# Optimization experiments

Measured on AMD Instinct MI355X. Metric: run time of the kernel, lower is better.

The kernel has to match this reference:

```python
import jax, jax.numpy as jnp
import numpy as np

B, S, E, H = 4, 8192, 1024, 16
D = E // H  # head_dim = 64


def setup_inputs() -> dict:
    key = jax.random.key(0)
    ks = jax.random.split(key, 6)
    x = jax.random.normal(ks[0], (B, S, E), dtype=jnp.float32)
    key_padding_mask = jax.random.randint(ks[1], (B, S), 0, 2).astype(jnp.bool_)
    scale = 1.0 / np.sqrt(E)
    Wq = jax.random.normal(ks[2], (E, E), dtype=jnp.float32) * scale
    Wk = jax.random.normal(ks[3], (E, E), dtype=jnp.float32) * scale
    Wv = jax.random.normal(ks[4], (E, E), dtype=jnp.float32) * scale
    Wo = jax.random.normal(ks[5], (E, E), dtype=jnp.float32) * scale
    return {"x": x, "key_padding_mask": key_padding_mask,
            "Wq": Wq, "Wk": Wk, "Wv": Wv, "Wo": Wo}


def reference(x, key_padding_mask, Wq, Wk, Wv, Wo):
    b, s, _ = x.shape
    # torch Linear (no bias): y = x @ W.T
    Q = (x @ Wq.T).reshape(b, s, H, D).transpose(0, 2, 1, 3)  # (b,h,s,d)
    K = (x @ Wk.T).reshape(b, s, H, D).transpose(0, 2, 1, 3)
    V = (x @ Wv.T).reshape(b, s, H, D).transpose(0, 2, 1, 3)
    Q = jax.nn.elu(Q) + 1.0
    K = jax.nn.elu(K) + 1.0
    mask = key_padding_mask[:, None, :, None]  # (b,1,s,1), True = padding
    K = jnp.where(mask, 0.0, K)
    V = jnp.where(mask, 0.0, V)
    # global KV summarization over sequence: (b,h,d,e)
    KV = jnp.einsum('bhsd,bhse->bhde', K, V)
    K_sum = K.sum(axis=2)  # (b,h,d)
    Z = 1.0 / (jnp.einsum('bhsd,bhd->bhs', Q, K_sum) + 1e-6)  # (b,h,s)
    out = jnp.einsum('bhsd,bhde->bhse', Q, KV) * Z[..., None]  # (b,h,s,e)
    out = out.transpose(0, 2, 1, 3).reshape(b, s, E)
    return out @ Wo.T
```

## Files before the change

### kernel.cpp

```cpp
#include <hip/hip_runtime.h>

#define NB 4
#define NS 8192
#define NE 1024
#define NH 16
#define ND 64
#define NM (NB*NS)
#define NKT 16

typedef __bf16 bf16x8 __attribute__((ext_vector_type(8)));
typedef float  f32x4  __attribute__((ext_vector_type(4)));
typedef unsigned short u16x8 __attribute__((ext_vector_type(8)));

__device__ __forceinline__ unsigned short f2bf(float f){
  unsigned int u = __float_as_uint(f);
  u += 0x7FFFu + ((u >> 16) & 1u);
  return (unsigned short)(u >> 16);
}
__device__ __forceinline__ float bf2f(unsigned short h){
  return __uint_as_float(((unsigned int)h) << 16);
}
__device__ __forceinline__ void gload16(const void* g, void* lds){
  __builtin_amdgcn_global_load_lds(
      (__attribute__((address_space(1))) unsigned int*)g,
      (__attribute__((address_space(3))) unsigned int*)lds, 16, 0, 0);
}

__global__ void mask_prep(const void* mraw, unsigned char* mask_u8){
  __shared__ int flag_s;
  if (threadIdx.x == 0) flag_s = 0;
  __syncthreads();
  const unsigned int* mi = (const unsigned int*)mraw;
  int bad = 0;
  for (int i = threadIdx.x; i < 4096; i += 256) bad |= (mi[i] > 1u) ? 1 : 0;
  if (bad) atomicOr(&flag_s, 1);
  __syncthreads();
  const int isbyte = flag_s;
  const unsigned char* mb = (const unsigned char*)mraw;
  int stride = gridDim.x * blockDim.x;
  for (int i = blockIdx.x*blockDim.x + threadIdx.x; i < NM; i += stride)
    mask_u8[i] = isbyte ? (unsigned char)(mb[i] != 0) : (unsigned char)(mi[i] != 0);
}

struct CastJobs {
  const float* src[5];
  unsigned short* dst[5];
  int n4[5];
};

__global__ __launch_bounds__(256) void castk(CastJobs J){
  int j = blockIdx.y;
  const float* s = J.src[j];
  unsigned short* d = J.dst[j];
  int n4 = J.n4[j];
  int stride = gridDim.x * blockDim.x;
  for (int i = blockIdx.x*blockDim.x + threadIdx.x; i < n4; i += stride){
    float4 v = *(const float4*)(s + (long)i*4);
    ushort4 o;
    o.x = f2bf(v.x); o.y = f2bf(v.y); o.z = f2bf(v.z); o.w = f2bf(v.w);
    *(ushort4*)(d + (long)i*4) = o;
  }
}

__global__ __launch_bounds__(512, 2) void gemm256(
    const unsigned short* __restrict__ A,
    const unsigned short* __restrict__ W0,
    const unsigned short* __restrict__ W1,
    const unsigned short* __restrict__ W2,
    unsigned short* __restrict__ O0,
    unsigned short* __restrict__ O1,
    unsigned short* __restrict__ O2,
    float* __restrict__ OF,
    const unsigned char* __restrict__ mask,
    int modeSel)
{
  __shared__ __align__(16) unsigned short As[2*256*64];
  __shared__ __align__(16) unsigned short Bs[2*256*64];

  const int mode = (modeSel < 0) ? (int)blockIdx.y : modeSel;
  const unsigned short* Bw = (mode==0) ? W0 : (mode==1) ? W1 : (mode==2) ? W2 : W0;
  unsigned short* Obf = (mode==0) ? O0 : (mode==1) ? O1 : O2;

  const int nwg = (int)gridDim.x;
  const int bx  = (int)blockIdx.x;
  const int swz = (bx & 7) * (nwg >> 3) + (bx >> 3);
  const long m0 = (long)(swz >> 2) * 256;
  const int  n0 = (swz & 3) * 256;

  const int tid = (int)threadIdx.x;
  const int l   = tid & 63;
  const int wv  = tid >> 6;
  const int wr  = wv >> 2;
  const int wc  = wv & 3;
  const int l15 = l & 15;
  const int lhi = l >> 4;
  const int swz8 = (l & 7) * 8;

  const int srow = wv*16 + (l >> 3);
  const int scol = ((l & 7) * 8) ^ ((l >> 3) << 3);

  auto stageA = [&](int st, int h){
    if (st >= NKT) return;
    const long col = (long)st*64 + scol;
    #pragma unroll
    for (int is = 0; is < 2; ++is)
      gload16(A + (m0 + h*128 + srow + is*8)*NE + col,
              &As[(st & 1)*16384 + h*8192 + (wv*2 + is)*512]);
  };
  auto stageB = [&](int st, int h){
    if (st >= NKT) return;
    const long col = (long)st*64 + scol;
    #pragma unroll
    for (int is = 0; is < 2; ++is)
      gload16(Bw + (long)(n0 + h*128 + srow + is*8)*NE + col,
              &Bs[(st & 1)*16384 + h*8192 + (wv*2 + is)*512]);
  };

  auto lda = [&](int buf, int mi, int ks)->bf16x8 {
    const int row = wr*128 + mi*16 + l15;
    const int col = (ks*32 + lhi*8) ^ swz8;
    return *(const bf16x8*)&As[buf*16384 + row*64 + col];
  };
  auto ldb = [&](int buf, int ni, int ks)->bf16x8 {
    const int row = wc*64 + ni*16 + l15;
    const int col = (ks*32 + lhi*8) ^ swz8;
    return *(const bf16x8*)&Bs[buf*16384 + row*64 + col];
  };

  f32x4 acc[8][4];
  #pragma unroll
  for (int i=0;i<8;++i)
    #pragma unroll
    for (int j=0;j<4;++j)
      acc[i][j] = (f32x4){0.f,0.f,0.f,0.f};

  stageA(0,0); stageA(0,1); stageB(0,0); stageB(0,1);
  stageA(1,0); stageA(1,1); stageB(1,0); stageB(1,1);
  asm volatile("s_waitcnt vmcnt(8)" ::: "memory");
  __builtin_amdgcn_s_barrier();

  bf16x8 a0[4][2], a1[4][2], b0[2][2], b1[2][2];

  #pragma unroll 2
  for (int kt = 0; kt < NKT; ++kt){
    const int buf = kt & 1;

    #pragma unroll
    for (int i=0;i<4;++i){ a0[i][0]=lda(buf,i,0); a0[i][1]=lda(buf,i,1); }
    #pragma unroll
    for (int j=0;j<2;++j){ b0[j][0]=ldb(buf,j,0); b0[j][1]=ldb(buf,j,1); }
    asm volatile("s_waitcnt lgkmcnt(0)" ::: "memory");
    __builtin_amdgcn_sched_barrier(0);
    __builtin_amdgcn_s_setprio(1);
    #pragma unroll
    for (int ks=0;ks<2;++ks)
      #pragma unroll
      for (int i=0;i<4;++i)
        #pragma unroll
        for (int j=0;j<2;++j)
          acc[i][j] = __builtin_amdgcn_mfma_f32_16x16x32_bf16(a0[i][ks], b0[j][ks], acc[i][j], 0,0,0);
    __builtin_amdgcn_s_setprio(0);
    __builtin_amdgcn_s_barrier();

    #pragma unroll
    for (int i=0;i<4;++i){ a1[i][0]=lda(buf,4+i,0); a1[i][1]=lda(buf,4+i,1); }
    asm volatile("s_waitcnt lgkmcnt(0)" ::: "memory");
    __builtin_amdgcn_sched_barrier(0);
    __builtin_amdgcn_s_setprio(1);
    #pragma unroll
    for (int ks=0;ks<2;++ks)
      #pragma unroll
      for (int i=0;i<4;++i)
        #pragma unroll
        for (int j=0;j<2;++j)
          acc[4+i][j] = __builtin_amdgcn_mfma_f32_16x16x32_bf16(a1[i][ks], b0[j][ks], acc[4+i][j], 0,0,0);
    __builtin_amdgcn_s_setprio(0);
    __builtin_amdgcn_s_barrier();

    #pragma unroll
    for (int j=0;j<2;++j){ b1[j][0]=ldb(buf,2+j,0); b1[j][1]=ldb(buf,2+j,1); }
    stageA(kt+2, 0); stageA(kt+2, 1);
    asm volatile("s_waitcnt lgkmcnt(0)" ::: "memory");
    __builtin_amdgcn_sched_barrier(0);
    __builtin_amdgcn_s_setprio(1);
    #pragma unroll
    for (int ks=0;ks<2;++ks)
      #pragma unroll
      for (int i=0;i<4;++i)
        #pragma unroll
        for (int j=0;j<2;++j)
          acc[4+i][2+j] = __builtin_amdgcn_mfma_f32_16x16x32_bf16(a1[i][ks], b1[j][ks], acc[4+i][2+j], 0,0,0);
    __builtin_amdgcn_s_setprio(0);
    __builtin_amdgcn_s_barrier();

    stageB(kt+2, 0); stageB(kt+2, 1);
    __builtin_amdgcn_sched_barrier(0);
    __builtin_amdgcn_s_setprio(1);
    #pragma unroll
    for (int ks=0;ks<2;++ks)
      #pragma unroll
      for (int i=0;i<4;++i)
        #pragma unroll
        for (int j=0;j<2;++j)
          acc[i][2+j] = __builtin_amdgcn_mfma_f32_16x16x32_bf16(a0[i][ks], b1[j][ks], acc[i][2+j], 0,0,0);
    __builtin_amdgcn_s_setprio(0);
    if (kt < NKT-2)       asm volatile("s_waitcnt vmcnt(8)" ::: "memory");
    else if (kt == NKT-2) asm volatile("s_waitcnt vmcnt(0)" ::: "memory");
    __builtin_amdgcn_s_barrier();
  }

  #pragma unroll
  for (int mi=0;mi<8;++mi){
    #pragma unroll
    for (int r=0;r<4;++r){
      const long mg = m0 + wr*128 + mi*16 + lhi*4 + r;
      const bool mz = (mode==1 || mode==2) ? (mask[mg] != 0) : false;
      #pragma unroll
      for (int ni=0;ni<4;++ni){
        const int ng = n0 + wc*64 + ni*16 + l15;
        float v = acc[mi][ni][r];
        if (mode==0 || mode==1) v = (v > 0.f) ? (v + 1.f) : __expf(v);
        if (mz) v = 0.f;
        if (mode==3) OF[mg*NE + ng] = v;
        else         Obf[mg*NE + ng] = f2bf(v);
      }
    }
  }
}

__global__ __launch_bounds__(256) void kv_reduce(const unsigned short* __restrict__ K,
                                                 const unsigned short* __restrict__ V,
                                                 float* __restrict__ part){
  __shared__ float lds[2*64*68 + 192];
  float* Ksf = lds;
  float* Vsf = lds + 64*68;
  float* kcorner = lds + 2*64*68;

  const int bid = blockIdx.x;
  const int bh = bid >> 5;
  const int chunk = bid & 31;
  const int b = bh >> 4, h = bh & 15;
  const int t = threadIdx.x, w = t >> 6, l = t & 63;
  const int dg = l & 7, eg = l >> 3;
  const int d0 = dg*8, e0 = eg*8;
  const long base = ((long)b*NS + (long)chunk*256)*NE + h*ND;

  f32x4 acc[8][2];
  #pragma unroll
  for (int j=0;j<8;++j){ acc[j][0]=(f32x4){0,0,0,0}; acc[j][1]=(f32x4){0,0,0,0}; }
  f32x4 ksa = (f32x4){0,0,0,0}, ksb = (f32x4){0,0,0,0};

  for (int sc = 0; sc < 4; ++sc){
    if (sc) __syncthreads();
    const long rbase = base + (long)sc*64*NE;
    #pragma unroll
    for (int p = 0; p < 2; ++p){
      const int g = p*256 + t;
      const int row = g >> 3, cg = (g & 7)*8;
      u16x8 ku = *(const u16x8*)(K + rbase + (long)row*NE + cg);
      u16x8 vu = *(const u16x8*)(V + rbase + (long)row*NE + cg);
      #pragma unroll
      for (int j=0;j<8;++j){
        Ksf[row*68 + cg + j] = bf2f(ku[j]);
        Vsf[row*68 + cg + j] = bf2f(vu[j]);
      }
    }
    __syncthreads();
    #pragma unroll 2
    for (int i = 0; i < 16; ++i){
      const int r = w*16 + i;
      f32x4 k0 = *(const f32x4*)&Ksf[r*68 + d0];
      f32x4 k1 = *(const f32x4*)&Ksf[r*68 + d0 + 4];
      f32x4 v0 = *(const f32x4*)&Vsf[r*68 + e0];
      f32x4 v1 = *(const f32x4*)&Vsf[r*68 + e0 + 4];
      #pragma unroll
      for (int j=0;j<4;++j){
        acc[j][0]   += k0[j]*v0;  acc[j][1]   += k0[j]*v1;
        acc[4+j][0] += k1[j]*v0;  acc[4+j][1] += k1[j]*v1;
      }
      if (eg == 0){ ksa += k0; ksb += k1; }
    }
  }

  __syncthreads();
  if (w >= 1 && eg == 0){
    *(f32x4*)&kcorner[(w-1)*64 + d0]     = ksa;
    *(f32x4*)&kcorner[(w-1)*64 + d0 + 4] = ksb;
  }
  if (w >= 2){
    float* reg = (w==2) ? Ksf : Vsf;
    #pragma unroll
    for (int j=0;j<8;++j)
      #pragma unroll
      for (int q=0;q<2;++q)
        *(f32x4*)&reg[l*68 + (j*2+q)*4] = acc[j][q];
  }
  __syncthreads();
  if (w < 2){
    float* reg = (w==0) ? Ksf : Vsf;
    #pragma unroll
    for (int j=0;j<8;++j)
      #pragma unroll
      for (int q=0;q<2;++q)
        acc[j][q] += *(const f32x4*)&reg[l*68 + (j*2+q)*4];
  }
  __syncthreads();
  if (w == 1){
    #pragma unroll
    for (int j=0;j<8;++j)
      #pragma unroll
      for (int q=0;q<2;++q)
        *(f32x4*)&Ksf[l*68 + (j*2+q)*4] = acc[j][q];
  }
  __syncthreads();
  if (w == 0){
    #pragma unroll
    for (int j=0;j<8;++j)
      #pragma unroll
      for (int q=0;q<2;++q)
        acc[j][q] += *(const f32x4*)&Ksf[l*68 + (j*2+q)*4];
    float* po = part + (long)(bh*32 + chunk)*4160;
    #pragma unroll
    for (int j=0;j<8;++j)
      #pragma unroll
      for (int q=0;q<2;++q)
        *(f32x4*)&po[(d0 + j)*64 + e0 + q*4] = acc[j][q];
    if (eg == 0){
      #pragma unroll
      for (int i=0;i<3;++i){
        ksa += *(const f32x4*)&kcorner[i*64 + d0];
        ksb += *(const f32x4*)&kcorner[i*64 + d0 + 4];
      }
      *(f32x4*)&po[4096 + d0]     = ksa;
      *(f32x4*)&po[4096 + d0 + 4] = ksb;
    }
  }
}

__global__ __launch_bounds__(256) void kv_finish(const float* __restrict__ part,
                                                 unsigned short* __restrict__ KVfrag){
  __shared__ float KVf[64*65 + 32];
  const int bh = blockIdx.x, t = threadIdx.x;
  const float* pb = part + (long)bh*32*4160;

  #pragma unroll
  for (int p = 0; p < 4; ++p){
    int g = p*256 + t;
    f32x4 s = (f32x4){0.f,0.f,0.f,0.f};
    for (int c = 0; c < 32; ++c) s += *(const f32x4*)&pb[c*4160 + g*4];
    int d = g >> 4, e = (g & 15)*4;
    KVf[d*65 + e+0] = s[0];
    KVf[d*65 + e+1] = s[1];
    KVf[d*65 + e+2] = s[2];
    KVf[d*65 + e+3] = s[3];
  }
  if (t < 16){
    f32x4 s = (f32x4){0.f,0.f,0.f,0.f};
    for (int c = 0; c < 32; ++c) s += *(const f32x4*)&pb[c*4160 + 4096 + t*4];
    #pragma unroll
    for (int j=0;j<4;++j) KVf[(t*4+j)*65 + 64] = s[j];
  }
  __syncthreads();

  for (int idx = t; idx < 10240; idx += 256){
    int j   = idx & 7;
    int lfr = (idx >> 3) & 63;
    int grp = idx >> 9;
    int nt  = grp % 5, ks = grp / 5;
    int kk  = (ks & 1)*32 + (lfr >> 4)*8 + j;
    int n   = nt*16 + (lfr & 15);
    float v = (n <= 64) ? KVf[kk*65 + n] : 0.f;
    unsigned short hi = f2bf(v);
    unsigned short o  = (ks >> 1) ? f2bf(v - bf2f(hi)) : hi;
    KVfrag[(long)bh*10240 + idx] = o;
  }
}

__global__ __launch_bounds__(256) void attn_mfma(const unsigned short* __restrict__ Q,
                                                 const unsigned short* __restrict__ KVfrag,
                                                 unsigned short* __restrict__ attn){
  __shared__ unsigned short Qs[256*64];
  const int bid = blockIdx.x;
  const int bh = bid >> 5, chunk = bid & 31;
  const int b = bh >> 4, h = bh & 15;
  const int t = threadIdx.x, w = t >> 6, l = t & 63;
  const int l15 = l & 15, lhi = l >> 4;
  const long row0 = (long)b*NS + chunk*256;

  const int srccol = ((l & 7) ^ (l >> 3)) * 8;
  #pragma unroll
  for (int c = 0; c < 8; ++c){
    const int r = w*64 + c*8 + (l >> 3);
    gload16(Q + (row0 + r)*NE + h*ND + srccol, &Qs[(w*8 + c)*512]);
  }

  bf16x8 bf[4][5];
  #pragma unroll
  for (int ks=0; ks<4; ++ks)
    #pragma unroll
    for (int nt=0; nt<5; ++nt)
      bf[ks][nt] = *(const bf16x8*)(KVfrag + (long)bh*10240 + (ks*5+nt)*512 + l*8);

  __syncthreads();

  const int swz = (l15 & 7) << 4;
  const char* qbase = (const char*)&Qs[w*4096];

  #pragma unroll
  for (int rt=0; rt<4; ++rt){
    const int rb = (rt*16 + l15)*128;
    bf16x8 a0 = *(const bf16x8*)(qbase + rb + ((lhi*16) ^ swz));
    bf16x8 a1 = *(const bf16x8*)(qbase + rb + ((64 + lhi*16) ^ swz));
    f32x4 acc[5];
    #pragma unroll
    for (int nt=0; nt<5; ++nt){
      acc[nt] = (f32x4){0.f,0.f,0.f,0.f};
      acc[nt] = __builtin_amdgcn_mfma_f32_16x16x32_bf16(a0, bf[0][nt], acc[nt], 0,0,0);
      acc[nt] = __builtin_amdgcn_mfma_f32_16x16x32_bf16(a1, bf[1][nt], acc[nt], 0,0,0);
      acc[nt] = __builtin_amdgcn_mfma_f32_16x16x32_bf16(a0, bf[2][nt], acc[nt], 0,0,0);
      acc[nt] = __builtin_amdgcn_mfma_f32_16x16x32_bf16(a1, bf[3][nt], acc[nt], 0,0,0);
    }
    float dv[4];
    #pragma unroll
    for (int e=0;e<4;++e){
      float d = __shfl(acc[4][e], l & 48, 64);
      dv[e] = 1.f / (d + 1e-6f);
    }
    #pragma unroll
    for (int nt=0; nt<4; ++nt){
      #pragma unroll
      for (int e=0;e<4;++e){
        const int row = rt*16 + lhi*4 + e;
        const int cb  = (nt*16 + l15)*2;
        Qs[w*4096 + ((row*128 + (cb ^ ((row & 7) << 4))) >> 1)] = f2bf(acc[nt][e] * dv[e]);
      }
    }
  }

  asm volatile("s_waitcnt lgkmcnt(0)" ::: "memory");
  #pragma unroll
  for (int c=0;c<8;++c){
    const int r = c*8 + (l >> 3);
    bf16x8 vv = *(const bf16x8*)((const char*)&Qs[w*4096] + r*128 + ((((l&7) ^ (l>>3))) << 4));
    *(bf16x8*)(attn + (row0 + w*64 + r)*NE + h*ND + (l&7)*8) = vv;
  }
}

extern "C" void kernel_launch(void* const* d_in, const int* in_sizes, int n_in,
                              void* d_out, int out_size, void* d_ws, size_t ws_size,
                              hipStream_t stream){
  (void)in_sizes; (void)n_in; (void)out_size; (void)ws_size;
  const float* x    = (const float*)d_in[0];
  const void*  mraw = d_in[1];
  const float* Wq   = (const float*)d_in[2];
  const float* Wk   = (const float*)d_in[3];
  const float* Wv   = (const float*)d_in[4];
  const float* Wo   = (const float*)d_in[5];
  float* out = (float*)d_out;
  char* ws = (char*)d_ws;

  unsigned short* xb  = (unsigned short*)(ws + 0L);
  unsigned short* Wqb = (unsigned short*)(ws + 67108864L);
  unsigned short* Wkb = (unsigned short*)(ws + 69206016L);
  unsigned short* Wvb = (unsigned short*)(ws + 71303168L);
  unsigned short* Wob = (unsigned short*)(ws + 73400320L);
  unsigned short* Qb  = (unsigned short*)(ws + 75497472L);
  unsigned short* Kb  = (unsigned short*)(ws + 142606336L);
  unsigned short* Vb  = (unsigned short*)(ws + 209715200L);
  unsigned short* KVfrag = (unsigned short*)(ws + 276824064L);
  unsigned char* mask_u8 = (unsigned char*)(ws + 278462464L);
  float* part = (float*)xb;

  mask_prep<<<32, 256, 0, stream>>>(mraw, mask_u8);

  CastJobs J;
  J.src[0]=x;  J.dst[0]=xb;  J.n4[0]=NM*NE/4;
  J.src[1]=Wq; J.dst[1]=Wqb; J.n4[1]=NE*NE/4;
  J.src[2]=Wk; J.dst[2]=Wkb; J.n4[2]=NE*NE/4;
  J.src[3]=Wv; J.dst[3]=Wvb; J.n4[3]=NE*NE/4;
  J.src[4]=Wo; J.dst[4]=Wob; J.n4[4]=NE*NE/4;
  castk<<<dim3(2048,5), 256, 0, stream>>>(J);

  gemm256<<<dim3(512,3), 512, 0, stream>>>(xb, Wqb, Wkb, Wvb,
                                           Qb, Kb, Vb, nullptr, mask_u8, -1);

  kv_reduce<<<dim3(2048), 256, 0, stream>>>(Kb, Vb, part);
  kv_finish<<<dim3(64), 256, 0, stream>>>(part, KVfrag);

  attn_mfma<<<dim3(2048), 256, 0, stream>>>(Qb, KVfrag, xb);

  gemm256<<<dim3(512,1), 512, 0, stream>>>(xb, Wob, Wob, Wob,
                                           nullptr, nullptr, nullptr, out, mask_u8, 3);
}
```

Baseline: 469.0 us.

## Fuse Q projection GEMM with linear-attention apply into one kernel

The Q projection is removed from the batched QKV GEMM and moved into a new kernel that computes Q tiles, applies elu+1, stages them in shared memory, and multiplies by the per-head KV fragment in the same block. Each wave's 64-column slice matches one head, so the normalized attention output is written directly and the Q buffer never goes through global memory. This avoids a full write and reread of Q plus one kernel launch. The cost is more register and shared-memory pressure in the GEMM epilogue, and the attention step can no longer overlap with other blocks of a separate launch.

Result: faster. 456.0 us (median of 2 runs) (-2.8%).

```diff
diff --git a/kernel.cpp b/kernel.cpp
--- a/kernel.cpp
+++ b/kernel.cpp
@@ -64,10 +64,8 @@
 
 __global__ __launch_bounds__(512, 2) void gemm256(
     const unsigned short* __restrict__ A,
-    const unsigned short* __restrict__ W0,
     const unsigned short* __restrict__ W1,
     const unsigned short* __restrict__ W2,
-    unsigned short* __restrict__ O0,
     unsigned short* __restrict__ O1,
     unsigned short* __restrict__ O2,
     float* __restrict__ OF,
@@ -77,9 +75,9 @@
   __shared__ __align__(16) unsigned short As[2*256*64];
   __shared__ __align__(16) unsigned short Bs[2*256*64];
 
-  const int mode = (modeSel < 0) ? (int)blockIdx.y : modeSel;
-  const unsigned short* Bw = (mode==0) ? W0 : (mode==1) ? W1 : (mode==2) ? W2 : W0;
-  unsigned short* Obf = (mode==0) ? O0 : (mode==1) ? O1 : O2;
+  const int mode = (modeSel < 0) ? (int)blockIdx.y + 1 : modeSel;
+  const unsigned short* Bw = (mode==1) ? W1 : (mode==2) ? W2 : W1;
+  unsigned short* Obf = (mode==1) ? O1 : O2;
 
   const int nwg = (int)gridDim.x;
   const int bx  = (int)blockIdx.x;
@@ -219,12 +217,221 @@
       for (int ni=0;ni<4;++ni){
         const int ng = n0 + wc*64 + ni*16 + l15;
         float v = acc[mi][ni][r];
-        if (mode==0 || mode==1) v = (v > 0.f) ? (v + 1.f) : __expf(v);
+        if (mode==1) v = (v > 0.f) ? (v + 1.f) : __expf(v);
         if (mz) v = 0.f;
         if (mode==3) OF[mg*NE + ng] = v;
         else         Obf[mg*NE + ng] = f2bf(v);
       }
     }
+  }
+}
+
+__global__ __launch_bounds__(512, 2) void gemm_q_attn(
+    const unsigned short* __restrict__ A,
+    const unsigned short* __restrict__ Wq,
+    const unsigned short* __restrict__ KVfrag,
+    unsigned short* __restrict__ attnb)
+{
+  __shared__ __align__(16) unsigned short As[2*256*64];
+  __shared__ __align__(16) unsigned short Bs[2*256*64];
+
+  const int nwg = (int)gridDim.x;
+  const int bx  = (int)blockIdx.x;
+  const int swz = (bx & 7) * (nwg >> 3) + (bx >> 3);
+  const long m0 = (long)(swz >> 2) * 256;
+  const int  n0 = (swz & 3) * 256;
+
+  const int tid = (int)threadIdx.x;
+  const int l   = tid & 63;
+  const int wv  = tid >> 6;
+  const int wr  = wv >> 2;
+  const int wc  = wv & 3;
+  const int l15 = l & 15;
+  const int lhi = l >> 4;
+  const int swz8 = (l & 7) * 8;
+
+  const int srow = wv*16 + (l >> 3);
+  const int scol = ((l & 7) * 8) ^ ((l >> 3) << 3);
+
+  auto stageA = [&](int st, int h){
+    if (st >= NKT) return;
+    const long col = (long)st*64 + scol;
+    #pragma unroll
+    for (int is = 0; is < 2; ++is)
+      gload16(A + (m0 + h*128 + srow + is*8)*NE + col,
+              &As[(st & 1)*16384 + h*8192 + (wv*2 + is)*512]);
+  };
+  auto stageB = [&](int st, int h){
+    if (st >= NKT) return;
+    const long col = (long)st*64 + scol;
+    #pragma unroll
+    for (int is = 0; is < 2; ++is)
+      gload16(Wq + (long)(n0 + h*128 + srow + is*8)*NE + col,
+              &Bs[(st & 1)*16384 + h*8192 + (wv*2 + is)*512]);
+  };
+
+  auto lda = [&](int buf, int mi, int ks)->bf16x8 {
+    const int row = wr*128 + mi*16 + l15;
+    const int col = (ks*32 + lhi*8) ^ swz8;
+    return *(const bf16x8*)&As[buf*16384 + row*64 + col];
+  };
+  auto ldb = [&](int buf, int ni, int ks)->bf16x8 {
+    const int row = wc*64 + ni*16 + l15;
+    const int col = (ks*32 + lhi*8) ^ swz8;
+    return *(const bf16x8*)&Bs[buf*16384 + row*64 + col];
+  };
+
+  f32x4 acc[8][4];
+  #pragma unroll
+  for (int i=0;i<8;++i)
+    #pragma unroll
+    for (int j=0;j<4;++j)
+      acc[i][j] = (f32x4){0.f,0.f,0.f,0.f};
+
+  stageA(0,0); stageA(0,1); stageB(0,0); stageB(0,1);
+  stageA(1,0); stageA(1,1); stageB(1,0); stageB(1,1);
+  asm volatile("s_waitcnt vmcnt(8)" ::: "memory");
+  __builtin_amdgcn_s_barrier();
+
+  bf16x8 a0[4][2], a1[4][2], b0[2][2], b1[2][2];
+
+  #pragma unroll 2
+  for (int kt = 0; kt < NKT; ++kt){
+    const int buf = kt & 1;
+
+    #pragma unroll
+    for (int i=0;i<4;++i){ a0[i][0]=lda(buf,i,0); a0[i][1]=lda(buf,i,1); }
+    #pragma unroll
+    for (int j=0;j<2;++j){ b0[j][0]=ldb(buf,j,0); b0[j][1]=ldb(buf,j,1); }
+    asm volatile("s_waitcnt lgkmcnt(0)" ::: "memory");
+    __builtin_amdgcn_sched_barrier(0);
+    __builtin_amdgcn_s_setprio(1);
+    #pragma unroll
+    for (int ks=0;ks<2;++ks)
+      #pragma unroll
+      for (int i=0;i<4;++i)
+        #pragma unroll
+        for (int j=0;j<2;++j)
+          acc[i][j] = __builtin_amdgcn_mfma_f32_16x16x32_bf16(a0[i][ks], b0[j][ks], acc[i][j], 0,0,0);
+    __builtin_amdgcn_s_setprio(0);
+    __builtin_amdgcn_s_barrier();
+
+    #pragma unroll
+    for (int i=0;i<4;++i){ a1[i][0]=lda(buf,4+i,0); a1[i][1]=lda(buf,4+i,1); }
+    asm volatile("s_waitcnt lgkmcnt(0)" ::: "memory");
+    __builtin_amdgcn_sched_barrier(0);
+    __builtin_amdgcn_s_setprio(1);
+    #pragma unroll
+    for (int ks=0;ks<2;++ks)
+      #pragma unroll
+      for (int i=0;i<4;++i)
+        #pragma unroll
+        for (int j=0;j<2;++j)
+          acc[4+i][j] = __builtin_amdgcn_mfma_f32_16x16x32_bf16(a1[i][ks], b0[j][ks], acc[4+i][j], 0,0,0);
+    __builtin_amdgcn_s_setprio(0);
+    __builtin_amdgcn_s_barrier();
+
+    #pragma unroll
+    for (int j=0;j<2;++j){ b1[j][0]=ldb(buf,2+j,0); b1[j][1]=ldb(buf,2+j,1); }
+    stageA(kt+2, 0); stageA(kt+2, 1);
+    asm volatile("s_waitcnt lgkmcnt(0)" ::: "memory");
+    __builtin_amdgcn_sched_barrier(0);
+    __builtin_amdgcn_s_setprio(1);
+    #pragma unroll
+    for (int ks=0;ks<2;++ks)
+      #pragma unroll
+      for (int i=0;i<4;++i)
+        #pragma unroll
+        for (int j=0;j<2;++j)
+          acc[4+i][2+j] = __builtin_amdgcn_mfma_f32_16x16x32_bf16(a1[i][ks], b1[j][ks], acc[4+i][2+j], 0,0,0);
+    __builtin_amdgcn_s_setprio(0);
+    __builtin_amdgcn_s_barrier();
+
+    stageB(kt+2, 0); stageB(kt+2, 1);
+    __builtin_amdgcn_sched_barrier(0);
+    __builtin_amdgcn_s_setprio(1);
+    #pragma unroll
+    for (int ks=0;ks<2;++ks)
+      #pragma unroll
+      for (int i=0;i<4;++i)
+        #pragma unroll
+        for (int j=0;j<2;++j)
+          acc[i][2+j] = __builtin_amdgcn_mfma_f32_16x16x32_bf16(a0[i][ks], b1[j][ks], acc[i][2+j], 0,0,0);
+    __builtin_amdgcn_s_setprio(0);
+    if (kt < NKT-2)       asm volatile("s_waitcnt vmcnt(8)" ::: "memory");
+    else if (kt == NKT-2) asm volatile("s_waitcnt vmcnt(0)" ::: "memory");
+    __builtin_amdgcn_s_barrier();
+  }
+
+  const int b  = (int)(m0 >> 13);
+  const int h  = (swz & 3)*4 + wc;
+  const long bh = (long)(b*16 + h);
+  unsigned short* pool = (wv < 4) ? &As[wv*8192] : &Bs[(wv-4)*8192];
+
+  #pragma unroll
+  for (int mi=0;mi<8;++mi){
+    #pragma unroll
+    for (int r=0;r<4;++r){
+      const int row = mi*16 + lhi*4 + r;
+      #pragma unroll
+      for (int ni=0;ni<4;++ni){
+        float v = acc[mi][ni][r];
+        v = (v > 0.f) ? (v + 1.f) : __expf(v);
+        const int colb = (ni*16 + l15)*2;
+        *(unsigned short*)((char*)pool + row*128 + (colb ^ ((row & 7) << 4))) = f2bf(v);
+      }
+    }
+  }
+
+  bf16x8 bfv[4][5];
+  #pragma unroll
+  for (int ks=0; ks<4; ++ks)
+    #pragma unroll
+    for (int nt=0; nt<5; ++nt)
+      bfv[ks][nt] = *(const bf16x8*)(KVfrag + bh*10240 + (ks*5+nt)*512 + l*8);
+
+  asm volatile("s_waitcnt lgkmcnt(0)" ::: "memory");
+  __builtin_amdgcn_sched_barrier(0);
+
+  const int swzb = (l15 & 7) << 4;
+  #pragma unroll
+  for (int rt=0; rt<8; ++rt){
+    const int rb = (rt*16 + l15)*128;
+    bf16x8 qa0 = *(const bf16x8*)((const char*)pool + rb + ((lhi*16) ^ swzb));
+    bf16x8 qa1 = *(const bf16x8*)((const char*)pool + rb + ((64 + lhi*16) ^ swzb));
+    f32x4 at[5];
+    #pragma unroll
+    for (int nt=0; nt<5; ++nt){
+      at[nt] = (f32x4){0.f,0.f,0.f,0.f};
+      at[nt] = __builtin_amdgcn_mfma_f32_16x16x32_bf16(qa0, bfv[0][nt], at[nt], 0,0,0);
+      at[nt] = __builtin_amdgcn_mfma_f32_16x16x32_bf16(qa1, bfv[1][nt], at[nt], 0,0,0);
+      at[nt] = __builtin_amdgcn_mfma_f32_16x16x32_bf16(qa0, bfv[2][nt], at[nt], 0,0,0);
+      at[nt] = __builtin_amdgcn_mfma_f32_16x16x32_bf16(qa1, bfv[3][nt], at[nt], 0,0,0);
+    }
+    float dv[4];
+    #pragma unroll
+    for (int e=0;e<4;++e){
+      float d = __shfl(at[4][e], l & 48, 64);
+      dv[e] = 1.f / (d + 1e-6f);
+    }
+    #pragma unroll
+    for (int nt=0; nt<4; ++nt){
+      #pragma unroll
+      for (int e=0;e<4;++e){
+        const int row = rt*16 + lhi*4 + e;
+        const int colb = (nt*16 + l15)*2;
+        *(unsigned short*)((char*)pool + row*128 + (colb ^ ((row & 7) << 4))) = f2bf(at[nt][e] * dv[e]);
+      }
+    }
+  }
+
+  asm volatile("s_waitcnt lgkmcnt(0)" ::: "memory");
+  __builtin_amdgcn_sched_barrier(0);
+  #pragma unroll
+  for (int c=0;c<16;++c){
+    const int r = c*8 + (l >> 3);
+    bf16x8 vv = *(const bf16x8*)((const char*)pool + r*128 + ((((l&7) ^ (r & 7))) << 4));
+    *(bf16x8*)(attnb + (m0 + wr*128 + r)*NE + h*ND + (l&7)*8) = vv;
   }
 }
 
@@ -373,76 +580,6 @@
     unsigned short hi = f2bf(v);
     unsigned short o  = (ks >> 1) ? f2bf(v - bf2f(hi)) : hi;
     KVfrag[(long)bh*10240 + idx] = o;
-  }
-}
-
-__global__ __launch_bounds__(256) void attn_mfma(const unsigned short* __restrict__ Q,
-                                                 const unsigned short* __restrict__ KVfrag,
-                                                 unsigned short* __restrict__ attn){
-  __shared__ unsigned short Qs[256*64];
-  const int bid = blockIdx.x;
-  const int bh = bid >> 5, chunk = bid & 31;
-  const int b = bh >> 4, h = bh & 15;
-  const int t = threadIdx.x, w = t >> 6, l = t & 63;
-  const int l15 = l & 15, lhi = l >> 4;
-  const long row0 = (long)b*NS + chunk*256;
-
-  const int srccol = ((l & 7) ^ (l >> 3)) * 8;
-  #pragma unroll
-  for (int c = 0; c < 8; ++c){
-    const int r = w*64 + c*8 + (l >> 3);
-    gload16(Q + (row0 + r)*NE + h*ND + srccol, &Qs[(w*8 + c)*512]);
-  }
-
-  bf16x8 bf[4][5];
-  #pragma unroll
-  for (int ks=0; ks<4; ++ks)
-    #pragma unroll
-    for (int nt=0; nt<5; ++nt)
-      bf[ks][nt] = *(const bf16x8*)(KVfrag + (long)bh*10240 + (ks*5+nt)*512 + l*8);
-
-  __syncthreads();
-
-  const int swz = (l15 & 7) << 4;
-  const char* qbase = (const char*)&Qs[w*4096];
-
-  #pragma unroll
-  for (int rt=0; rt<4; ++rt){
-    const int rb = (rt*16 + l15)*128;
-    bf16x8 a0 = *(const bf16x8*)(qbase + rb + ((lhi*16) ^ swz));
-    bf16x8 a1 = *(const bf16x8*)(qbase + rb + ((64 + lhi*16) ^ swz));
-    f32x4 acc[5];
-    #pragma unroll
-    for (int nt=0; nt<5; ++nt){
-      acc[nt] = (f32x4){0.f,0.f,0.f,0.f};
-      acc[nt] = __builtin_amdgcn_mfma_f32_16x16x32_bf16(a0, bf[0][nt], acc[nt], 0,0,0);
-      acc[nt] = __builtin_amdgcn_mfma_f32_16x16x32_bf16(a1, bf[1][nt], acc[nt], 0,0,0);
-      acc[nt] = __builtin_amdgcn_mfma_f32_16x16x32_bf16(a0, bf[2][nt], acc[nt], 0,0,0);
-      acc[nt] = __builtin_amdgcn_mfma_f32_16x16x32_bf16(a1, bf[3][nt], acc[nt], 0,0,0);
-    }
-    float dv[4];
-    #pragma unroll
-    for (int e=0;e<4;++e){
-      float d = __shfl(acc[4][e], l & 48, 64);
-      dv[e] = 1.f / (d + 1e-6f);
-    }
-    #pragma unroll
-    for (int nt=0; nt<4; ++nt){
-      #pragma unroll
-      for (int e=0;e<4;++e){
-        const int row = rt*16 + lhi*4 + e;
-        const int cb  = (nt*16 + l15)*2;
-        Qs[w*4096 + ((row*128 + (cb ^ ((row & 7) << 4))) >> 1)] = f2bf(acc[nt][e] * dv[e]);
-      }
-    }
-  }
-
-  asm volatile("s_waitcnt lgkmcnt(0)" ::: "memory");
-  #pragma unroll
-  for (int c=0;c<8;++c){
-    const int r = c*8 + (l >> 3);
-    bf16x8 vv = *(const bf16x8*)((const char*)&Qs[w*4096] + r*128 + ((((l&7) ^ (l>>3))) << 4));
-    *(bf16x8*)(attn + (row0 + w*64 + r)*NE + h*ND + (l&7)*8) = vv;
   }
 }
 
@@ -469,7 +606,8 @@
   unsigned short* Vb  = (unsigned short*)(ws + 209715200L);
   unsigned short* KVfrag = (unsigned short*)(ws + 276824064L);
   unsigned char* mask_u8 = (unsigned char*)(ws + 278462464L);
-  float* part = (float*)xb;
+  float* part = (float*)Qb;
+  unsigned short* attnb = Qb;
 
   mask_prep<<<32, 256, 0, stream>>>(mraw, mask_u8);
 
@@ -481,14 +619,12 @@
   J.src[4]=Wo; J.dst[4]=Wob; J.n4[4]=NE*NE/4;
   castk<<<dim3(2048,5), 256, 0, stream>>>(J);
 
-  gemm256<<<dim3(512,3), 512, 0, stream>>>(xb, Wqb, Wkb, Wvb,
-                                           Qb, Kb, Vb, nullptr, mask_u8, -1);
+  gemm256<<<dim3(512,2), 512, 0, stream>>>(xb, Wkb, Wvb, Kb, Vb, nullptr, mask_u8, -1);
 
   kv_reduce<<<dim3(2048), 256, 0, stream>>>(Kb, Vb, part);
   kv_finish<<<dim3(64), 256, 0, stream>>>(part, KVfrag);
 
-  attn_mfma<<<dim3(2048), 256, 0, stream>>>(Qb, KVfrag, xb);
-
-  gemm256<<<dim3(512,1), 512, 0, stream>>>(xb, Wob, Wob, Wob,
-                                           nullptr, nullptr, nullptr, out, mask_u8, 3);
-}
+  gemm_q_attn<<<dim3(512), 512, 0, stream>>>(xb, Wqb, KVfrag, attnb);
+
+  gemm256<<<dim3(512,1), 512, 0, stream>>>(attnb, Wob, Wob, nullptr, nullptr, out, mask_u8, 3);
+}
```
